# Optimization experiments

Hardware: AMD Instinct MI355X
Metric: run time of the kernel (lower is better)

## Reference

```python
import jax, jax.numpy as jnp
import numpy as np

B, L, C, H, O = 2048, 128, 32, 64, 16
N_SUB = 2  # fixed RK4 substeps per knot interval (stands in for torchdiffeq adaptive solver)


def hermite_coeffs(x, t):
    """torchcde.hermite_cubic_coefficients_with_backward_differences.
    x: (B, L, D), t: (L,) -> coeffs (B, L-1, 4*D) packed [a, b, 2c, 3d]."""
    dt = (t[1:] - t[:-1])[None, :, None]            # (1, L-1, 1)
    secants = (x[:, 1:] - x[:, :-1]) / dt           # (B, L-1, D)
    derivs = jnp.concatenate([secants[:, :1], secants], axis=1)  # backward diffs, first repeated
    x0, x1 = x[:, :-1], x[:, 1:]
    d0, d1 = derivs[:, :-1], derivs[:, 1:]
    delta = x1 - x0
    a = x0
    b = d0
    two_c = 2.0 * (3.0 * delta / dt - 2.0 * d0 - d1) / dt
    three_d = 3.0 * (-2.0 * delta / dt + d0 + d1) / (dt * dt)
    return jnp.concatenate([a, b, two_c, three_d], axis=-1)


def setup_inputs() -> dict:
    key = jax.random.key(0)
    ks = jax.random.split(key, 8)
    t = jnp.arange(L, dtype=jnp.float32)
    # coherent random control path -> spline coeffs (as torchcde would produce)
    path = jnp.cumsum(jax.random.normal(ks[0], (B, L, C), jnp.float32) * 0.1, axis=1)
    coeffs = hermite_coeffs(path, t)
    def lin(k, fan_in, fan_out):
        return jax.random.normal(k, (fan_in, fan_out), jnp.float32) / np.float32(np.sqrt(fan_in))
    return {
        "coeffs": coeffs,
        "t": t,
        "W_init": lin(ks[1], C, H), "b_init": jnp.zeros((H,), jnp.float32),
        "W1": lin(ks[2], H, 2), "b1": jnp.zeros((2,), jnp.float32),
        "W2": lin(ks[3], 2, H * C), "b2": jnp.zeros((H * C,), jnp.float32),
        "W_read": lin(ks[4], H, O), "b_read": jnp.zeros((O,), jnp.float32),
    }


def reference(coeffs, t, W_init, b_init, W1, b1, W2, b2, W_read, b_read):
    a, b, two_c, three_d = jnp.split(coeffs, 4, axis=-1)  # each (B, L-1, C)

    # X(interval[0]) = a of first interval
    X0 = a[:, 0]                                   # (B, C)
    z0 = X0 @ W_init + b_init                      # (B, H); dropout p=0 is a no-op

    def f(z):  # CDEFunc: (B,H) -> (B,H,C)
        h1 = jax.nn.relu(z @ W1 + b1)
        g = jnp.tanh(h1 @ W2 + b2)
        return g.reshape(z.shape[0], H, C)

    def g(z, bi, ci, di, s):  # f(z) @ dX/dt(s)
        dXdt = bi + ci * s + di * (s * s)          # (B, C)
        return jnp.einsum('bhc,bc->bh', f(z), dXdt)

    def interval_step(z, xs):
        bi, ci, di, dti = xs
        hstep = dti / N_SUB
        def sub(z, j):
            s = j * hstep
            k1 = g(z, bi, ci, di, s)
            k2 = g(z + 0.5 * hstep * k1, bi, ci, di, s + 0.5 * hstep)
            k3 = g(z + 0.5 * hstep * k2, bi, ci, di, s + 0.5 * hstep)
            k4 = g(z + hstep * k3, bi, ci, di, s + hstep)
            z = z + (hstep / 6.0) * (k1 + 2.0 * k2 + 2.0 * k3 + k4)
            return z, None
        z, _ = jax.lax.scan(sub, z, jnp.arange(N_SUB, dtype=jnp.float32))
        return z, z

    dt = t[1:] - t[:-1]                            # (L-1,)
    xs = (jnp.moveaxis(b, 1, 0), jnp.moveaxis(two_c, 1, 0), jnp.moveaxis(three_d, 1, 0), dt)
    _, z_seq = jax.lax.scan(interval_step, z0, xs)  # (L-1, B, H)

    z_T = jnp.moveaxis(jnp.concatenate([z0[None], z_seq], axis=0), 0, 1)  # (B, L, H)
    z_T = jnp.tanh(z_T)
    pred_y = z_T @ W_read + b_read                 # (B, L, O)
    new_coeffs = hermite_coeffs(pred_y, t)         # (B, L-1, 4*O)
    return pred_y, new_coeffs
```

## Files before the change

### kernel.cpp

```cpp
#include <hip/hip_runtime.h>
#include <cstdint>
#include <cstddef>

constexpr int Bn = 2048, Ln = 128, Cn = 32, Hn = 64, On = 16;
constexpr int NIv = Ln - 1;
constexpr float K2 = 2.885390081777927f;

typedef float v2f __attribute__((ext_vector_type(2)));

__device__ __forceinline__ float fexp2(float x) {
#if __has_builtin(__builtin_amdgcn_exp2f)
  return __builtin_amdgcn_exp2f(x);
#else
  float r; asm("v_exp_f32 %0, %1" : "=v"(r) : "v"(x)); return r;
#endif
}
__device__ __forceinline__ float frcpf(float x) {
#if __has_builtin(__builtin_amdgcn_rcpf)
  return __builtin_amdgcn_rcpf(x);
#else
  float r; asm("v_rcp_f32 %0, %1" : "=v"(r) : "v"(x)); return r;
#endif
}
__device__ __forceinline__ float tanh_fast(float x) {
  float e = fexp2(K2 * x);
  return fmaf(-2.0f, frcpf(e + 1.0f), 1.0f);
}

__device__ __forceinline__ v2f pk_fma(v2f a, v2f b, v2f c) {
  v2f d;
  asm("v_pk_fma_f32 %0, %1, %2, %3" : "=v"(d) : "v"(a), "v"(b), "v"(c));
  return d;
}

template<int CTRL>
__device__ __forceinline__ float dpp_addstep(float p) {
  int q = __builtin_amdgcn_update_dpp(0, __float_as_int(p), CTRL, 0xF, 0xF, true);
  return p + __int_as_float(q);
}
__device__ __forceinline__ float dpp_rowsum16(float p) {
  p = dpp_addstep<0xB1>(p);
  p = dpp_addstep<0x4E>(p);
  p = dpp_addstep<0x141>(p);
  p = dpp_addstep<0x140>(p);
  return p;
}
__device__ __forceinline__ float lane4_total(float p) {
  float s0 = __int_as_float(__builtin_amdgcn_readlane(__float_as_int(p), 0));
  float s1 = __int_as_float(__builtin_amdgcn_readlane(__float_as_int(p), 16));
  float s2 = __int_as_float(__builtin_amdgcn_readlane(__float_as_int(p), 32));
  float s3 = __int_as_float(__builtin_amdgcn_readlane(__float_as_int(p), 48));
  return (s0 + s1) + (s2 + s3);
}

#define REP8(M) M(0) M(1) M(2) M(3) M(4) M(5) M(6) M(7)

__global__ __launch_bounds__(256, 2) void ncde_scan_kernel(
    const float* __restrict__ coeffs, const float* __restrict__ t,
    const float* __restrict__ W_init, const float* __restrict__ b_init,
    const float* __restrict__ W1, const float* __restrict__ b1,
    const float* __restrict__ W2, const float* __restrict__ b2,
    float* __restrict__ zt)
{
  __shared__ float sdx[4][5][32];
  const int wv = threadIdx.x >> 6;
  const int lane = threadIdx.x & 63;
  const int b = (blockIdx.x << 2) | wv;
  float* const sdxw = &sdx[wv][0][0];

  const float w10 = W1[2 * lane], w11 = W1[2 * lane + 1];
  const float sb0 = b1[0], sb1 = b1[1];

#define DECLW(g) v2f w20a##g, w20b##g, w21a##g, w21b##g, ba##g, bb##g;
  REP8(DECLW)
  {
    const float* W2a = W2 + lane * 32;
    const float* W2b = W2 + 2048 + lane * 32;
    const float* b2a = b2 + lane * 32;
#define LOADW(g) { \
      const float4 x0 = *(const float4*)(W2a + 4 * (g)); \
      const float4 x1 = *(const float4*)(W2b + 4 * (g)); \
      const float4 x2 = *(const float4*)(b2a + 4 * (g)); \
      w20a##g = (v2f){x0.x * K2, x0.y * K2}; w20b##g = (v2f){x0.z * K2, x0.w * K2}; \
      w21a##g = (v2f){x1.x * K2, x1.y * K2}; w21b##g = (v2f){x1.z * K2, x1.w * K2}; \
      ba##g   = (v2f){x2.x * K2, x2.y * K2}; bb##g   = (v2f){x2.z * K2, x2.w * K2}; }
    REP8(LOADW)
  }

  const float* cb0 = coeffs + (size_t)b * NIv * 128;
  if (lane < 32) sdxw[lane] = cb0[lane];
  __builtin_amdgcn_wave_barrier();
  float z = b_init[lane];
#pragma unroll 4
  for (int c = 0; c < 32; ++c)
    z = fmaf(sdxw[c], W_init[(c << 6) + lane], z);
  zt[(size_t)b * Ln * Hn + lane] = tanh_fast(z);

#pragma unroll 1
  for (int i = 0; i < NIv; ++i) {
    const float* cb = cb0 + (size_t)i * 128;
    const float dti = t[i + 1] - t[i];
    const float hst = 0.5f * dti;
    __builtin_amdgcn_wave_barrier();
    if (lane < 32) {
      const float bi = cb[32 + lane];
      const float ci = cb[64 + lane];
      const float di = cb[96 + lane];
      const float q = 0.25f * dti;
#pragma unroll
      for (int k = 0; k < 5; ++k) {
        const float s = q * (float)k;
        sdxw[k * 32 + lane] = fmaf(fmaf(di, s, ci), s, bi);
      }
    }
    __builtin_amdgcn_wave_barrier();

    float kacc = 0.0f, kprev = 0.0f;
#pragma unroll
    for (int j = 0; j < 2; ++j) {
      if (j == 1) { z = fmaf(hst * (1.0f / 6.0f), kacc, z); kacc = 0.0f; kprev = 0.0f; }
#pragma unroll
      for (int st = 0; st < 4; ++st) {
        const float cin = (st == 0) ? 0.0f : (st == 3) ? hst : 0.5f * hst;
        const float wgt = (st == 1 || st == 2) ? 2.0f : 1.0f;
        const int kidx = 2 * j + ((st + 1) >> 1);
        const float* dx = sdxw + kidx * 32;
        const float zs = fmaf(cin, kprev, z);
        float p0 = dpp_rowsum16(zs * w10);
        float p1 = dpp_rowsum16(zs * w11);
        const float h10 = fmaxf(lane4_total(p0) + sb0, 0.0f);
        const float h11 = fmaxf(lane4_total(p1) + sb1, 0.0f);
        const v2f hb0 = (v2f){h10, h10};
        const v2f hb1 = (v2f){h11, h11};
        float a0 = 0.0f, a1 = 0.0f, a2 = 0.0f, a3 = 0.0f;
#define GRP(g) { \
        const float4 d4 = *(const float4*)(dx + 4 * (g)); \
        const v2f u0 = pk_fma(w20a##g, hb0, pk_fma(w21a##g, hb1, ba##g)); \
        const v2f u1 = pk_fma(w20b##g, hb0, pk_fma(w21b##g, hb1, bb##g)); \
        const float e0 = fexp2(u0.x), e1 = fexp2(u0.y); \
        const float e2 = fexp2(u1.x), e3 = fexp2(u1.y); \
        const float r0 = frcpf(e0 + 1.0f), r1 = frcpf(e1 + 1.0f); \
        const float r2 = frcpf(e2 + 1.0f), r3 = frcpf(e3 + 1.0f); \
        a0 = fmaf(fmaf(-2.0f, r0, 1.0f), d4.x, a0); \
        a1 = fmaf(fmaf(-2.0f, r1, 1.0f), d4.y, a1); \
        a2 = fmaf(fmaf(-2.0f, r2, 1.0f), d4.z, a2); \
        a3 = fmaf(fmaf(-2.0f, r3, 1.0f), d4.w, a3); }
        REP8(GRP)
        const float acc = (a0 + a1) + (a2 + a3);
        kprev = acc;
        kacc = fmaf(wgt, acc, kacc);
      }
    }
    z = fmaf(hst * (1.0f / 6.0f), kacc, z);
    zt[((size_t)b * Ln + (i + 1)) * Hn + lane] = tanh_fast(z);
  }
}

#define SPX(l_, o_) (((l_) << 4) | (((o_) + (l_)) & 15))
#define SZX(l_, h_) (((l_) << 6) | (((h_) + (l_)) & 63))

__global__ __launch_bounds__(128, 2) void ncde_epilogue_kernel(
    const float* __restrict__ zt, const float* __restrict__ t,
    const float* __restrict__ W_read, const float* __restrict__ b_read,
    float* __restrict__ out)
{
  __shared__ float sW[Hn * On];
  __shared__ float sz[Ln * Hn];
  __shared__ float sp[Ln * On];
  __shared__ float st_[Ln];
  const int b = blockIdx.x;
  const int tid = threadIdx.x;

  for (int i2 = tid; i2 < Hn * On; i2 += 128) sW[i2] = W_read[i2];
  st_[tid] = t[tid];
  const float* zb = zt + (size_t)b * Ln * Hn;
#pragma unroll 1
  for (int r = 0; r < 16; ++r) {
    const int base = (r * 128 + tid) * 4;
    const float4 v = *(const float4*)(zb + base);
    const int l = base >> 6, h = base & 63;
    sz[SZX(l, h + 0)] = v.x;
    sz[SZX(l, h + 1)] = v.y;
    sz[SZX(l, h + 2)] = v.z;
    sz[SZX(l, h + 3)] = v.w;
  }
  __syncthreads();

  float acc0[On];
#pragma unroll
  for (int o = 0; o < On; ++o) acc0[o] = b_read[o];
#pragma unroll 2
  for (int h = 0; h < Hn; ++h) {
    const float zv = sz[SZX(tid, h)];
#pragma unroll
    for (int o = 0; o < On; ++o) acc0[o] = fmaf(zv, sW[h * On + o], acc0[o]);
  }
  float* po = out + ((size_t)b * Ln + tid) * On;
#pragma unroll
  for (int o = 0; o < On; ++o) sp[SPX(tid, o)] = acc0[o];
#pragma unroll
  for (int o4 = 0; o4 < 4; ++o4) {
    float4 v = make_float4(acc0[4*o4], acc0[4*o4+1], acc0[4*o4+2], acc0[4*o4+3]);
    *(float4*)(po + 4 * o4) = v;
  }
  __syncthreads();

  float* cbo = out + (size_t)Bn * Ln * On + (size_t)b * NIv * 64;
#pragma unroll 1
  for (int r = 0; r < 16; ++r) {
    const int item = r * 128 + tid;
    if (item < NIv * On) {
      const int i = item >> 4, o = item & 15;
      const float p0 = sp[SPX(i, o)], p1 = sp[SPX(i + 1, o)];
      const float rdt = frcpf(st_[i + 1] - st_[i]);
      const float si = (p1 - p0) * rdt;
      float d0;
      if (i == 0) d0 = si;
      else d0 = (p0 - sp[SPX(i - 1, o)]) * frcpf(st_[i] - st_[i - 1]);
      const float d1 = si;
      float* cc = cbo + (size_t)i * 64 + o;
      cc[0]  = p0;
      cc[16] = d0;
      cc[32] = 2.0f * (3.0f * si - 2.0f * d0 - d1) * rdt;
      cc[48] = 3.0f * (d0 + d1 - 2.0f * si) * (rdt * rdt);
    }
  }
}

extern "C" void kernel_launch(void* const* d_in, const int* in_sizes, int n_in,
                              void* d_out, int out_size, void* d_ws, size_t ws_size,
                              hipStream_t stream) {
  const float* coeffs = (const float*)d_in[0];
  const float* t      = (const float*)d_in[1];
  const float* W_init = (const float*)d_in[2];
  const float* b_init = (const float*)d_in[3];
  const float* W1     = (const float*)d_in[4];
  const float* b1     = (const float*)d_in[5];
  const float* W2     = (const float*)d_in[6];
  const float* b2     = (const float*)d_in[7];
  const float* W_read = (const float*)d_in[8];
  const float* b_read = (const float*)d_in[9];
  float* out = (float*)d_out;
  float* zt  = (float*)d_ws;

  ncde_scan_kernel<<<dim3(Bn / 4), dim3(256), 0, stream>>>(
      coeffs, t, W_init, b_init, W1, b1, W2, b2, zt);
  ncde_epilogue_kernel<<<dim3(Bn), dim3(128), 0, stream>>>(
      zt, t, W_read, b_read, out);
}
```

Before: 1.305 ms.

## Split each batch element's channel sum across two waves with LDS weights

Each batch element's RK4 scan now runs on two waves instead of one. Each wave evaluates 16 of the 32 control channels, and the two partial sums are combined through shared memory with a block barrier at every stage. The W2/b2 weights move from registers into shared memory, and the launch bound is raised to 4 blocks per CU, so twice as many waves are resident to hide the latency of the serial dependency chain. The cost is per-stage block synchronisation, extra LDS weight loads, and the W1 reduction now computed redundantly in both waves.

```diff
diff --git a/kernel.cpp b/kernel.cpp
--- a/kernel.cpp
+++ b/kernel.cpp
@@ -5,8 +5,6 @@
 constexpr int Bn = 2048, Ln = 128, Cn = 32, Hn = 64, On = 16;
 constexpr int NIv = Ln - 1;
 constexpr float K2 = 2.885390081777927f;
-
-typedef float v2f __attribute__((ext_vector_type(2)));
 
 __device__ __forceinline__ float fexp2(float x) {
 #if __has_builtin(__builtin_amdgcn_exp2f)
@@ -27,12 +25,6 @@
   return fmaf(-2.0f, frcpf(e + 1.0f), 1.0f);
 }
 
-__device__ __forceinline__ v2f pk_fma(v2f a, v2f b, v2f c) {
-  v2f d;
-  asm("v_pk_fma_f32 %0, %1, %2, %3" : "=v"(d) : "v"(a), "v"(b), "v"(c));
-  return d;
-}
-
 template<int CTRL>
 __device__ __forceinline__ float dpp_addstep(float p) {
   int q = __builtin_amdgcn_update_dpp(0, __float_as_int(p), CTRL, 0xF, 0xF, true);
@@ -53,67 +45,73 @@
   return (s0 + s1) + (s2 + s3);
 }
 
-#define REP8(M) M(0) M(1) M(2) M(3) M(4) M(5) M(6) M(7)
-
-__global__ __launch_bounds__(256, 2) void ncde_scan_kernel(
+__global__ __launch_bounds__(256, 4) void ncde_scan_kernel(
     const float* __restrict__ coeffs, const float* __restrict__ t,
     const float* __restrict__ W_init, const float* __restrict__ b_init,
     const float* __restrict__ W1, const float* __restrict__ b1,
     const float* __restrict__ W2, const float* __restrict__ b2,
     float* __restrict__ zt)
 {
-  __shared__ float sdx[4][5][32];
-  const int wv = threadIdx.x >> 6;
-  const int lane = threadIdx.x & 63;
-  const int b = (blockIdx.x << 2) | wv;
-  float* const sdxw = &sdx[wv][0][0];
+  __shared__ float2 sw[Cn * Hn];
+  __shared__ float  scc[Cn * Hn];
+  __shared__ alignas(16) float sdx[2][5][Cn];
+  __shared__ float  sacc[2][2][Hn];
+  const int tid  = threadIdx.x;
+  const int lane = tid & 63;
+  const int wv   = tid >> 6;
+  const int bi   = wv >> 1;
+  const int half = wv & 1;
+  const int b    = (blockIdx.x << 1) | bi;
+
+  for (int e = tid; e < Cn * Hn; e += 256) {
+    const int h = e >> 5, c = e & 31;
+    sw [c * Hn + h] = make_float2(K2 * W2[h * 32 + c], K2 * W2[2048 + h * 32 + c]);
+    scc[c * Hn + h] = K2 * b2[h * 32 + c];
+  }
 
   const float w10 = W1[2 * lane], w11 = W1[2 * lane + 1];
   const float sb0 = b1[0], sb1 = b1[1];
 
-#define DECLW(g) v2f w20a##g, w20b##g, w21a##g, w21b##g, ba##g, bb##g;
-  REP8(DECLW)
-  {
-    const float* W2a = W2 + lane * 32;
-    const float* W2b = W2 + 2048 + lane * 32;
-    const float* b2a = b2 + lane * 32;
-#define LOADW(g) { \
-      const float4 x0 = *(const float4*)(W2a + 4 * (g)); \
-      const float4 x1 = *(const float4*)(W2b + 4 * (g)); \
-      const float4 x2 = *(const float4*)(b2a + 4 * (g)); \
-      w20a##g = (v2f){x0.x * K2, x0.y * K2}; w20b##g = (v2f){x0.z * K2, x0.w * K2}; \
-      w21a##g = (v2f){x1.x * K2, x1.y * K2}; w21b##g = (v2f){x1.z * K2, x1.w * K2}; \
-      ba##g   = (v2f){x2.x * K2, x2.y * K2}; bb##g   = (v2f){x2.z * K2, x2.w * K2}; }
-    REP8(LOADW)
-  }
-
   const float* cb0 = coeffs + (size_t)b * NIv * 128;
-  if (lane < 32) sdxw[lane] = cb0[lane];
-  __builtin_amdgcn_wave_barrier();
+  if (half == 0 && lane < 32) sdx[bi][0][lane] = cb0[lane];
+  __syncthreads();
   float z = b_init[lane];
 #pragma unroll 4
   for (int c = 0; c < 32; ++c)
-    z = fmaf(sdxw[c], W_init[(c << 6) + lane], z);
-  zt[(size_t)b * Ln * Hn + lane] = tanh_fast(z);
+    z = fmaf(sdx[bi][0][c], W_init[(c << 6) + lane], z);
+  if (half == 0) zt[(size_t)b * Ln * Hn + lane] = tanh_fast(z);
+  __syncthreads();
+
+  const float2* swp  = sw  + (half << 4) * Hn + lane;
+  const float*  sccp = scc + (half << 4) * Hn + lane;
+  float* const saccw       = &sacc[bi][half][lane];
+  const float* const saccr = &sacc[bi][half ^ 1][lane];
 
 #pragma unroll 1
   for (int i = 0; i < NIv; ++i) {
     const float* cb = cb0 + (size_t)i * 128;
     const float dti = t[i + 1] - t[i];
     const float hst = 0.5f * dti;
-    __builtin_amdgcn_wave_barrier();
     if (lane < 32) {
-      const float bi = cb[32 + lane];
-      const float ci = cb[64 + lane];
-      const float di = cb[96 + lane];
+      const float bv = cb[32 + lane];
+      const float cv = cb[64 + lane];
+      const float dv = cb[96 + lane];
       const float q = 0.25f * dti;
-#pragma unroll
-      for (int k = 0; k < 5; ++k) {
-        const float s = q * (float)k;
-        sdxw[k * 32 + lane] = fmaf(fmaf(di, s, ci), s, bi);
+      if (half == 0) {
+#pragma unroll
+        for (int k = 0; k < 3; ++k) {
+          const float s = q * (float)k;
+          sdx[bi][k][lane] = fmaf(fmaf(dv, s, cv), s, bv);
+        }
+      } else {
+#pragma unroll
+        for (int k = 3; k < 5; ++k) {
+          const float s = q * (float)k;
+          sdx[bi][k][lane] = fmaf(fmaf(dv, s, cv), s, bv);
+        }
       }
     }
-    __builtin_amdgcn_wave_barrier();
+    __syncthreads();
 
     float kacc = 0.0f, kprev = 0.0f;
 #pragma unroll
@@ -124,35 +122,51 @@
         const float cin = (st == 0) ? 0.0f : (st == 3) ? hst : 0.5f * hst;
         const float wgt = (st == 1 || st == 2) ? 2.0f : 1.0f;
         const int kidx = 2 * j + ((st + 1) >> 1);
-        const float* dx = sdxw + kidx * 32;
+        const float* dxp = &sdx[bi][kidx][half << 4];
         const float zs = fmaf(cin, kprev, z);
-        float p0 = dpp_rowsum16(zs * w10);
-        float p1 = dpp_rowsum16(zs * w11);
+        const float p0 = dpp_rowsum16(zs * w10);
+        const float p1 = dpp_rowsum16(zs * w11);
         const float h10 = fmaxf(lane4_total(p0) + sb0, 0.0f);
         const float h11 = fmaxf(lane4_total(p1) + sb1, 0.0f);
-        const v2f hb0 = (v2f){h10, h10};
-        const v2f hb1 = (v2f){h11, h11};
         float a0 = 0.0f, a1 = 0.0f, a2 = 0.0f, a3 = 0.0f;
-#define GRP(g) { \
-        const float4 d4 = *(const float4*)(dx + 4 * (g)); \
-        const v2f u0 = pk_fma(w20a##g, hb0, pk_fma(w21a##g, hb1, ba##g)); \
-        const v2f u1 = pk_fma(w20b##g, hb0, pk_fma(w21b##g, hb1, bb##g)); \
-        const float e0 = fexp2(u0.x), e1 = fexp2(u0.y); \
-        const float e2 = fexp2(u1.x), e3 = fexp2(u1.y); \
-        const float r0 = frcpf(e0 + 1.0f), r1 = frcpf(e1 + 1.0f); \
-        const float r2 = frcpf(e2 + 1.0f), r3 = frcpf(e3 + 1.0f); \
-        a0 = fmaf(fmaf(-2.0f, r0, 1.0f), d4.x, a0); \
-        a1 = fmaf(fmaf(-2.0f, r1, 1.0f), d4.y, a1); \
-        a2 = fmaf(fmaf(-2.0f, r2, 1.0f), d4.z, a2); \
-        a3 = fmaf(fmaf(-2.0f, r3, 1.0f), d4.w, a3); }
-        REP8(GRP)
-        const float acc = (a0 + a1) + (a2 + a3);
+#pragma unroll
+        for (int g = 0; g < 4; ++g) {
+          const float4 d4 = *(const float4*)(dxp + 4 * g);
+          {
+            const float2 w = swp[(4 * g + 0) * Hn];
+            const float u = fmaf(w.x, h10, fmaf(w.y, h11, sccp[(4 * g + 0) * Hn]));
+            const float r = frcpf(fexp2(u) + 1.0f);
+            a0 = fmaf(fmaf(-2.0f, r, 1.0f), d4.x, a0);
+          }
+          {
+            const float2 w = swp[(4 * g + 1) * Hn];
+            const float u = fmaf(w.x, h10, fmaf(w.y, h11, sccp[(4 * g + 1) * Hn]));
+            const float r = frcpf(fexp2(u) + 1.0f);
+            a1 = fmaf(fmaf(-2.0f, r, 1.0f), d4.y, a1);
+          }
+          {
+            const float2 w = swp[(4 * g + 2) * Hn];
+            const float u = fmaf(w.x, h10, fmaf(w.y, h11, sccp[(4 * g + 2) * Hn]));
+            const float r = frcpf(fexp2(u) + 1.0f);
+            a2 = fmaf(fmaf(-2.0f, r, 1.0f), d4.z, a2);
+          }
+          {
+            const float2 w = swp[(4 * g + 3) * Hn];
+            const float u = fmaf(w.x, h10, fmaf(w.y, h11, sccp[(4 * g + 3) * Hn]));
+            const float r = frcpf(fexp2(u) + 1.0f);
+            a3 = fmaf(fmaf(-2.0f, r, 1.0f), d4.w, a3);
+          }
+        }
+        const float part = (a0 + a1) + (a2 + a3);
+        *saccw = part;
+        __syncthreads();
+        const float acc = part + *saccr;
         kprev = acc;
         kacc = fmaf(wgt, acc, kacc);
       }
     }
     z = fmaf(hst * (1.0f / 6.0f), kacc, z);
-    zt[((size_t)b * Ln + (i + 1)) * Hn + lane] = tanh_fast(z);
+    if (half == 0) zt[((size_t)b * Ln + (i + 1)) * Hn + lane] = tanh_fast(z);
   }
 }
 
@@ -243,7 +257,7 @@
   float* out = (float*)d_out;
   float* zt  = (float*)d_ws;
 
-  ncde_scan_kernel<<<dim3(Bn / 4), dim3(256), 0, stream>>>(
+  ncde_scan_kernel<<<dim3(Bn / 2), dim3(256), 0, stream>>>(
       coeffs, t, W_init, b_init, W1, b1, W2, b2, zt);
   ncde_epilogue_kernel<<<dim3(Bn), dim3(128), 0, stream>>>(
       zt, t, W_read, b_read, out);
```

New measurement: 1.654 ms. 1.27x slower.

## Fold tanh affine into precomputed dX sums, use scalar FMAs and one-wave blocks

Applied to the files above, without the earlier changes.

Rewrites tanh(u)*dx as dx - 2*rcp(exp+1)*dx, so the per-element '1-2r' FMA is dropped and replaced by a per-stage sum of dX/dt that is computed once per interval with full-wave DPP reductions. Packed v_pk_fma is replaced with scalar FMAs and the weights are pinned in registers. The scan kernel moves from 4-wave blocks to single-wave 64-thread blocks, and the cross-row reduction becomes DPP row broadcasts plus a single readlane. This adds three extra reductions per interval and changes the occupancy and scheduling profile, and the different rounding order slightly changes numerics.

```diff
diff --git a/kernel.cpp b/kernel.cpp
--- a/kernel.cpp
+++ b/kernel.cpp
@@ -5,8 +5,6 @@
 constexpr int Bn = 2048, Ln = 128, Cn = 32, Hn = 64, On = 16;
 constexpr int NIv = Ln - 1;
 constexpr float K2 = 2.885390081777927f;
-
-typedef float v2f __attribute__((ext_vector_type(2)));
 
 __device__ __forceinline__ float fexp2(float x) {
 #if __has_builtin(__builtin_amdgcn_exp2f)
@@ -27,51 +25,40 @@
   return fmaf(-2.0f, frcpf(e + 1.0f), 1.0f);
 }
 
-__device__ __forceinline__ v2f pk_fma(v2f a, v2f b, v2f c) {
-  v2f d;
-  asm("v_pk_fma_f32 %0, %1, %2, %3" : "=v"(d) : "v"(a), "v"(b), "v"(c));
-  return d;
-}
-
-template<int CTRL>
+template<int CTRL, int RMASK>
 __device__ __forceinline__ float dpp_addstep(float p) {
-  int q = __builtin_amdgcn_update_dpp(0, __float_as_int(p), CTRL, 0xF, 0xF, true);
+  int q = __builtin_amdgcn_update_dpp(0, __float_as_int(p), CTRL, RMASK, 0xF, true);
   return p + __int_as_float(q);
 }
-__device__ __forceinline__ float dpp_rowsum16(float p) {
-  p = dpp_addstep<0xB1>(p);
-  p = dpp_addstep<0x4E>(p);
-  p = dpp_addstep<0x141>(p);
-  p = dpp_addstep<0x140>(p);
-  return p;
-}
-__device__ __forceinline__ float lane4_total(float p) {
-  float s0 = __int_as_float(__builtin_amdgcn_readlane(__float_as_int(p), 0));
-  float s1 = __int_as_float(__builtin_amdgcn_readlane(__float_as_int(p), 16));
-  float s2 = __int_as_float(__builtin_amdgcn_readlane(__float_as_int(p), 32));
-  float s3 = __int_as_float(__builtin_amdgcn_readlane(__float_as_int(p), 48));
-  return (s0 + s1) + (s2 + s3);
+__device__ __forceinline__ float fullsum64(float p) {
+  p = dpp_addstep<0xB1, 0xF>(p);
+  p = dpp_addstep<0x4E, 0xF>(p);
+  p = dpp_addstep<0x141, 0xF>(p);
+  p = dpp_addstep<0x140, 0xF>(p);
+  p = dpp_addstep<0x142, 0xA>(p);
+  p = dpp_addstep<0x143, 0xC>(p);
+  return __int_as_float(__builtin_amdgcn_readlane(__float_as_int(p), 63));
 }
 
 #define REP8(M) M(0) M(1) M(2) M(3) M(4) M(5) M(6) M(7)
 
-__global__ __launch_bounds__(256, 2) void ncde_scan_kernel(
+__global__ __launch_bounds__(64, 2) void ncde_scan_kernel(
     const float* __restrict__ coeffs, const float* __restrict__ t,
     const float* __restrict__ W_init, const float* __restrict__ b_init,
     const float* __restrict__ W1, const float* __restrict__ b1,
     const float* __restrict__ W2, const float* __restrict__ b2,
     float* __restrict__ zt)
 {
-  __shared__ float sdx[4][5][32];
-  const int wv = threadIdx.x >> 6;
-  const int lane = threadIdx.x & 63;
-  const int b = (blockIdx.x << 2) | wv;
-  float* const sdxw = &sdx[wv][0][0];
+  __shared__ alignas(16) float sdx[5][32];
+  const int lane = threadIdx.x;
+  const int b = blockIdx.x;
 
   const float w10 = W1[2 * lane], w11 = W1[2 * lane + 1];
   const float sb0 = b1[0], sb1 = b1[1];
 
-#define DECLW(g) v2f w20a##g, w20b##g, w21a##g, w21b##g, ba##g, bb##g;
+#define DECLW(g) float Ax##g, Ay##g, Az##g, Aw##g, \
+                       Bx##g, By##g, Bz##g, Bw##g, \
+                       Cx##g, Cy##g, Cz##g, Cw##g;
   REP8(DECLW)
   {
     const float* W2a = W2 + lane * 32;
@@ -81,19 +68,23 @@
       const float4 x0 = *(const float4*)(W2a + 4 * (g)); \
       const float4 x1 = *(const float4*)(W2b + 4 * (g)); \
       const float4 x2 = *(const float4*)(b2a + 4 * (g)); \
-      w20a##g = (v2f){x0.x * K2, x0.y * K2}; w20b##g = (v2f){x0.z * K2, x0.w * K2}; \
-      w21a##g = (v2f){x1.x * K2, x1.y * K2}; w21b##g = (v2f){x1.z * K2, x1.w * K2}; \
-      ba##g   = (v2f){x2.x * K2, x2.y * K2}; bb##g   = (v2f){x2.z * K2, x2.w * K2}; }
+      Ax##g = x0.x * K2; Ay##g = x0.y * K2; Az##g = x0.z * K2; Aw##g = x0.w * K2; \
+      Bx##g = x1.x * K2; By##g = x1.y * K2; Bz##g = x1.z * K2; Bw##g = x1.w * K2; \
+      Cx##g = x2.x * K2; Cy##g = x2.y * K2; Cz##g = x2.z * K2; Cw##g = x2.w * K2; }
     REP8(LOADW)
+#define PINW(g) asm("" : "+v"(Ax##g), "+v"(Ay##g), "+v"(Az##g), "+v"(Aw##g), \
+                         "+v"(Bx##g), "+v"(By##g), "+v"(Bz##g), "+v"(Bw##g), \
+                         "+v"(Cx##g), "+v"(Cy##g), "+v"(Cz##g), "+v"(Cw##g));
+    REP8(PINW)
   }
 
   const float* cb0 = coeffs + (size_t)b * NIv * 128;
-  if (lane < 32) sdxw[lane] = cb0[lane];
+  if (lane < 32) sdx[0][lane] = cb0[lane];
   __builtin_amdgcn_wave_barrier();
   float z = b_init[lane];
 #pragma unroll 4
   for (int c = 0; c < 32; ++c)
-    z = fmaf(sdxw[c], W_init[(c << 6) + lane], z);
+    z = fmaf(sdx[0][c], W_init[(c << 6) + lane], z);
   zt[(size_t)b * Ln * Hn + lane] = tanh_fast(z);
 
 #pragma unroll 1
@@ -101,18 +92,28 @@
     const float* cb = cb0 + (size_t)i * 128;
     const float dti = t[i + 1] - t[i];
     const float hst = 0.5f * dti;
+    const float q = 0.25f * dti;
+    const int lc = lane & 31;
+    const float bv = cb[32 + lc];
+    const float cv = cb[64 + lc];
+    const float dv = cb[96 + lc];
     __builtin_amdgcn_wave_barrier();
     if (lane < 32) {
-      const float bi = cb[32 + lane];
-      const float ci = cb[64 + lane];
-      const float di = cb[96 + lane];
-      const float q = 0.25f * dti;
 #pragma unroll
       for (int k = 0; k < 5; ++k) {
         const float s = q * (float)k;
-        sdxw[k * 32 + lane] = fmaf(fmaf(di, s, ci), s, bi);
+        sdx[k][lc] = fmaf(fmaf(dv, s, cv), s, bv);
       }
     }
+    const float Sb = fullsum64(bv);
+    const float Sc = fullsum64(cv);
+    const float Sd = fullsum64(dv);
+#define SUMK(s_) (0.5f * fmaf((s_), fmaf((s_), Sd, Sc), Sb))
+    const float sm0 = 0.5f * Sb;
+    const float sm1 = SUMK(q);
+    const float sm2 = SUMK(2.0f * q);
+    const float sm3 = SUMK(3.0f * q);
+    const float sm4 = SUMK(4.0f * q);
     __builtin_amdgcn_wave_barrier();
 
     float kacc = 0.0f, kprev = 0.0f;
@@ -124,29 +125,29 @@
         const float cin = (st == 0) ? 0.0f : (st == 3) ? hst : 0.5f * hst;
         const float wgt = (st == 1 || st == 2) ? 2.0f : 1.0f;
         const int kidx = 2 * j + ((st + 1) >> 1);
-        const float* dx = sdxw + kidx * 32;
+        const float smk = (kidx == 0) ? sm0 : (kidx == 1) ? sm1
+                        : (kidx == 2) ? sm2 : (kidx == 3) ? sm3 : sm4;
+        const float* dxp = &sdx[kidx][0];
         const float zs = fmaf(cin, kprev, z);
-        float p0 = dpp_rowsum16(zs * w10);
-        float p1 = dpp_rowsum16(zs * w11);
-        const float h10 = fmaxf(lane4_total(p0) + sb0, 0.0f);
-        const float h11 = fmaxf(lane4_total(p1) + sb1, 0.0f);
-        const v2f hb0 = (v2f){h10, h10};
-        const v2f hb1 = (v2f){h11, h11};
+        const float h10 = fmaxf(fullsum64(zs * w10) + sb0, 0.0f);
+        const float h11 = fmaxf(fullsum64(zs * w11) + sb1, 0.0f);
         float a0 = 0.0f, a1 = 0.0f, a2 = 0.0f, a3 = 0.0f;
 #define GRP(g) { \
-        const float4 d4 = *(const float4*)(dx + 4 * (g)); \
-        const v2f u0 = pk_fma(w20a##g, hb0, pk_fma(w21a##g, hb1, ba##g)); \
-        const v2f u1 = pk_fma(w20b##g, hb0, pk_fma(w21b##g, hb1, bb##g)); \
-        const float e0 = fexp2(u0.x), e1 = fexp2(u0.y); \
-        const float e2 = fexp2(u1.x), e3 = fexp2(u1.y); \
-        const float r0 = frcpf(e0 + 1.0f), r1 = frcpf(e1 + 1.0f); \
-        const float r2 = frcpf(e2 + 1.0f), r3 = frcpf(e3 + 1.0f); \
-        a0 = fmaf(fmaf(-2.0f, r0, 1.0f), d4.x, a0); \
-        a1 = fmaf(fmaf(-2.0f, r1, 1.0f), d4.y, a1); \
-        a2 = fmaf(fmaf(-2.0f, r2, 1.0f), d4.z, a2); \
-        a3 = fmaf(fmaf(-2.0f, r3, 1.0f), d4.w, a3); }
+        const float4 d4 = *(const float4*)(dxp + 4 * (g)); \
+        const float u0 = fmaf(Ax##g, h10, fmaf(Bx##g, h11, Cx##g)); \
+        const float u1 = fmaf(Ay##g, h10, fmaf(By##g, h11, Cy##g)); \
+        const float u2 = fmaf(Az##g, h10, fmaf(Bz##g, h11, Cz##g)); \
+        const float u3 = fmaf(Aw##g, h10, fmaf(Bw##g, h11, Cw##g)); \
+        const float r0 = frcpf(fexp2(u0) + 1.0f); \
+        const float r1 = frcpf(fexp2(u1) + 1.0f); \
+        const float r2 = frcpf(fexp2(u2) + 1.0f); \
+        const float r3 = frcpf(fexp2(u3) + 1.0f); \
+        a0 = fmaf(r0, d4.x, a0); \
+        a1 = fmaf(r1, d4.y, a1); \
+        a2 = fmaf(r2, d4.z, a2); \
+        a3 = fmaf(r3, d4.w, a3); }
         REP8(GRP)
-        const float acc = (a0 + a1) + (a2 + a3);
+        const float acc = fmaf(-2.0f, (a0 + a1) + (a2 + a3), smk);
         kprev = acc;
         kacc = fmaf(wgt, acc, kacc);
       }
@@ -243,7 +244,7 @@
   float* out = (float*)d_out;
   float* zt  = (float*)d_ws;
 
-  ncde_scan_kernel<<<dim3(Bn / 4), dim3(256), 0, stream>>>(
+  ncde_scan_kernel<<<dim3(Bn), dim3(64), 0, stream>>>(
       coeffs, t, W_init, b_init, W1, b1, W2, b2, zt);
   ncde_epilogue_kernel<<<dim3(Bn), dim3(128), 0, stream>>>(
       zt, t, W_read, b_read, out);
```

Measured after the change: 1.846 ms. +41.4%, slower.
